# Optimization experiments

Measured on AMD Instinct MI355X. Metric: run time of the kernel, lower is better.

Reference implementation:

```python
import jax, jax.numpy as jnp
import numpy as np
from jax import lax

B, C, H, W = 8, 128, 256, 256
OUT_CH = 64
IN_CH = C * 9  # 1152: module's in_channels = 9 * image channels (unfold with 3x3 kernel)


def setup_inputs() -> dict:
    key = jax.random.key(0)
    k1, k2, k3 = jax.random.split(key, 3)
    x = jax.random.normal(k1, (B, C, H, W), dtype=jnp.float32)
    style = jax.random.normal(k2, (B, IN_CH), dtype=jnp.float32)
    # learned parameter: torch.randn(out_channels, in_channels, 1, 1) -> store as (out, in)
    weight = jax.random.normal(k3, (OUT_CH, IN_CH), dtype=jnp.float32)
    return {"x": x, "style": style, "weight": weight}


def reference(x, style, weight):
    b, c, h, w = x.shape
    out_ch, in_ch = weight.shape  # in_ch == c * 9
    # unfold column ordering is (c, kh, kw), so the flattened weight is exactly a
    # 3x3 conv kernel: (out, c*9) -> (out, c, 3, 3)
    w33 = weight.reshape(out_ch, c, 3, 3)
    # style.view(B,1,in_ch,1,1) * weight -> per-sample modulated 3x3 kernels
    w_mod = style.reshape(b, 1, c, 3, 3) * w33[None]  # (B, out, c, 3, 3)

    def conv_one(xi, wi):
        # xi: (c, h, w), wi: (out, c, 3, 3); SAME padding matches padding=(1,1)
        return lax.conv_general_dilated(
            xi[None], wi, window_strides=(1, 1), padding="SAME",
            dimension_numbers=("NCHW", "OIHW", "NCHW"))[0]

    out = jax.vmap(conv_one)(x, w_mod)  # (B, out, h, w)
    return out
```

## Files before the change

### kernel.cpp

```cpp
#include <hip/hip_runtime.h>
#include <hip/hip_bf16.h>

#define BATCH 8
#define CIN   128
#define HH    256
#define WW    256
#define OUTC  64
#define INCH  1152
#define HW    (HH*WW)
#define WMOD_BYTES ((size_t)BATCH * 9 * OUTC * CIN * 2)

typedef __attribute__((ext_vector_type(8)))  short short8;
typedef __attribute__((ext_vector_type(4)))  float f32x4;
typedef __attribute__((ext_vector_type(16))) float f32x16;

__device__ __forceinline__ unsigned short bf16r(float f) {
    unsigned u = __builtin_bit_cast(unsigned, f);
    u += 0x7fffu + ((u >> 16) & 1u);
    return (unsigned short)(u >> 16);
}

__global__ void __launch_bounds__(256) wmod_kernel(const float* __restrict__ weight,
                                                   const float* __restrict__ style,
                                                   unsigned short* __restrict__ wmod) {
    int i = blockIdx.x * 256 + threadIdx.x;
    if (i >= BATCH * 9 * OUTC * CIN) return;
    int c    = i & (CIN - 1);
    int rest = i >> 7;
    int o    = rest & (OUTC - 1);
    int bt   = rest >> 6;
    int tap  = bt % 9;
    int b    = bt / 9;
    int k    = c * 9 + tap;
    wmod[i] = bf16r(weight[o * INCH + k] * style[b * INCH + k]);
}

#define PBAR()                                              \
    do {                                                    \
        asm volatile("s_waitcnt lgkmcnt(0)" ::: "memory");  \
        __builtin_amdgcn_sched_barrier(0);                  \
        __builtin_amdgcn_s_barrier();                       \
        __builtin_amdgcn_sched_barrier(0);                  \
    } while (0)

template <bool GW>
__global__ void __launch_bounds__(256, 2) conv10_kernel(
    const float* __restrict__ x,
    const unsigned short* __restrict__ wmod,
    const float* __restrict__ weight,
    const float* __restrict__ style,
    float* __restrict__ out)
{
    __shared__ __align__(16) unsigned short xs_sm[2][340 * 20];

    const int tid = threadIdx.x;
    const int bx  = blockIdx.x;
    const int b   = blockIdx.y;
    const int h0  = (bx >> 3) * 8;
    const int w0  = (bx & 7) * 32;

    const int wv  = tid >> 6;
    const int l31 = tid & 31;
    const int kh2 = (tid >> 5) & 1;

    const bool tv = tid < 200;
    const int tt  = tv ? tid : 0;
    const int cg  = tt / 100;
    const int rem = tt % 100;
    const int sr  = rem / 10;
    const int qw  = rem % 10;
    const int sh  = h0 - 1 + sr;
    const bool hok = tv && ((unsigned)sh < HH);
    const int wl  = w0 - 4 + qw * 4;
    const int wlc = min(max(wl, 0), WW - 4);
    const int colbase = wl - (w0 - 1);
    const float* xbase = x + ((size_t)(b * CIN + cg * 8)) * HW +
                         (hok ? sh : 0) * WW + wlc;

    f32x4  f[8];
    short8 A[9][2];

    auto loadG = [&](int chunk) {
        if (hok) {
#pragma unroll
            for (int j = 0; j < 8; ++j)
                f[j] = *(const f32x4*)(xbase + (size_t)(chunk * 16 + j) * HW);
        }
    };

    auto writeG = [&](unsigned short* buf) {
        if (tv) {
#pragma unroll
            for (int u = 0; u < 4; ++u) {
                int col = colbase + u;
                if (col >= 0 && col < 34) {
                    bool wok = hok && ((unsigned)(wl + u) < WW);
                    short8 sv;
#pragma unroll
                    for (int j = 0; j < 8; ++j)
                        sv[j] = wok ? (short)bf16r(f[j][u]) : (short)0;
                    int s = sr * 34 + col;
                    *(short8*)&buf[s * 20 + cg * 8] = sv;
                }
            }
        }
    };

    auto loadA = [&](int chunk) {
        if (GW) {
            const unsigned short* wb =
                wmod + ((size_t)(b * 9) * OUTC) * CIN + chunk * 16 + kh2 * 8;
#pragma unroll
            for (int tap = 0; tap < 9; ++tap)
#pragma unroll
                for (int mi = 0; mi < 2; ++mi)
                    A[tap][mi] = *(const short8*)(
                        wb + ((size_t)tap * OUTC + mi * 32 + l31) * CIN);
        } else {
#pragma unroll
            for (int tap = 0; tap < 9; ++tap)
#pragma unroll
                for (int mi = 0; mi < 2; ++mi) {
                    int o = mi * 32 + l31;
#pragma unroll
                    for (int j = 0; j < 8; ++j) {
                        int c = chunk * 16 + kh2 * 8 + j;
                        int k = c * 9 + tap;
                        A[tap][mi][j] = (short)bf16r(weight[o * INCH + k] *
                                                     style[b * INCH + k]);
                    }
                }
        }
    };

    f32x16 acc[2][2];
#pragma unroll
    for (int mi = 0; mi < 2; ++mi)
#pragma unroll
        for (int ni = 0; ni < 2; ++ni)
#pragma unroll
            for (int r = 0; r < 16; ++r) acc[mi][ni][r] = 0.f;

    auto compute = [&](const unsigned short* buf) {
#pragma unroll
        for (int kh = 0; kh < 3; ++kh)
#pragma unroll
            for (int kw = 0; kw < 3; ++kw) {
                const int tap = kh * 3 + kw;
                short8 Bv[2];
#pragma unroll
                for (int ni = 0; ni < 2; ++ni) {
                    int s = (2 * wv + ni + kh) * 34 + l31 + kw;
                    Bv[ni] = *(const short8*)&buf[s * 20 + kh2 * 8];
                }
#pragma unroll
                for (int mi = 0; mi < 2; ++mi)
#pragma unroll
                    for (int ni = 0; ni < 2; ++ni)
                        acc[mi][ni] = __builtin_amdgcn_mfma_f32_32x32x16_bf16(
                            A[tap][mi], Bv[ni], acc[mi][ni], 0, 0, 0);
            }
    };

    loadG(0);
    loadA(0);
    __builtin_amdgcn_sched_barrier(0);
    writeG(xs_sm[0]);
    PBAR();

#pragma unroll
    for (int k = 0; k < 8; ++k) {
        if (k < 7) loadG(k + 1);
        __builtin_amdgcn_sched_barrier(0);
        compute(xs_sm[k & 1]);
        __builtin_amdgcn_sched_barrier(0);
        if (k < 7) {
            loadA(k + 1);
            writeG(xs_sm[(k & 1) ^ 1]);
            PBAR();
        }
    }

    float* op = out + ((size_t)b * OUTC) * HW + w0 + l31;
#pragma unroll
    for (int mi = 0; mi < 2; ++mi)
#pragma unroll
        for (int ni = 0; ni < 2; ++ni) {
            int h = h0 + 2 * wv + ni;
#pragma unroll
            for (int r = 0; r < 16; ++r) {
                int o = mi * 32 + (r & 3) + 8 * (r >> 2) + 4 * kh2;
                op[(size_t)o * HW + h * WW] = acc[mi][ni][r];
            }
        }
}

extern "C" void kernel_launch(void* const* d_in, const int* in_sizes, int n_in,
                              void* d_out, int out_size, void* d_ws, size_t ws_size,
                              hipStream_t stream) {
    const float* x      = (const float*)d_in[0];
    const float* style  = (const float*)d_in[1];
    const float* weight = (const float*)d_in[2];
    float* out = (float*)d_out;

    const int wmod_total = BATCH * 9 * OUTC * CIN;

    if (ws_size >= WMOD_BYTES) {
        unsigned short* wmodp = (unsigned short*)d_ws;
        wmod_kernel<<<(wmod_total + 255) / 256, 256, 0, stream>>>(weight, style, wmodp);
        conv10_kernel<true><<<dim3(256, BATCH), 256, 0, stream>>>(
            x, wmodp, nullptr, nullptr, out);
    } else {
        conv10_kernel<false><<<dim3(256, BATCH), 256, 0, stream>>>(
            x, nullptr, weight, style, out);
    }
}
```

Baseline: 229.2 us.

## Pre-pack input to bf16 channel-grouped layout and stage tiles via direct global-to-LDS loads

Adds a repack kernel that converts x to bf16 in a layout of 8-channel groups per pixel, then a new conv kernel that stages halo tiles straight into LDS with global_load_lds, pointing out-of-bounds pixels at a zeroed buffer. This removes the per-iteration fp32 loads, bf16 conversion and LDS writes from the conv's inner loop, and relaxes the barrier wait so only older loads must finish. In exchange it needs a large workspace and an extra full pass over x: a 256 MB fp32 read plus a 128 MB bf16 write and re-read. That traffic may cost more than the conv saves.

```diff
diff --git a/kernel.cpp b/kernel.cpp
--- a/kernel.cpp
+++ b/kernel.cpp
@@ -8,17 +8,40 @@
 #define OUTC  64
 #define INCH  1152
 #define HW    (HH*WW)
+
+#define PLANE_PX   ((size_t)HH * WW)
+#define PLANE_B    (PLANE_PX * 16)
+#define XG_BYTES   ((size_t)BATCH * 16 * PLANE_B)
 #define WMOD_BYTES ((size_t)BATCH * 9 * OUTC * CIN * 2)
+#define Z_BYTES    64
 
 typedef __attribute__((ext_vector_type(8)))  short short8;
 typedef __attribute__((ext_vector_type(4)))  float f32x4;
+typedef __attribute__((ext_vector_type(2)))  float f32x2;
 typedef __attribute__((ext_vector_type(16))) float f32x16;
+typedef __attribute__((ext_vector_type(4)))  unsigned int u32x4;
 
 __device__ __forceinline__ unsigned short bf16r(float f) {
     unsigned u = __builtin_bit_cast(unsigned, f);
     u += 0x7fffu + ((u >> 16) & 1u);
     return (unsigned short)(u >> 16);
 }
+
+__device__ __forceinline__ void gload16(const void* src, void* dst_lds) {
+    __builtin_amdgcn_global_load_lds(
+        (const __attribute__((address_space(1))) unsigned int*)src,
+        (__attribute__((address_space(3))) unsigned int*)dst_lds,
+        16, 0, 0);
+}
+
+#define PBAR18()                                                        \
+    do {                                                                \
+        __builtin_amdgcn_sched_barrier(0);                              \
+        asm volatile("s_waitcnt vmcnt(18) lgkmcnt(0)" ::: "memory");    \
+        __builtin_amdgcn_sched_barrier(0);                              \
+        __builtin_amdgcn_s_barrier();                                   \
+        __builtin_amdgcn_sched_barrier(0);                              \
+    } while (0)
 
 __global__ void __launch_bounds__(256) wmod_kernel(const float* __restrict__ weight,
                                                    const float* __restrict__ style,
@@ -35,7 +58,159 @@
     wmod[i] = bf16r(weight[o * INCH + k] * style[b * INCH + k]);
 }
 
-#define PBAR()                                              \
+__global__ void __launch_bounds__(256) repack_kernel(const float* __restrict__ x,
+                                                     unsigned short* __restrict__ xG) {
+    const int w2 = blockIdx.x * 128 + (threadIdx.x & 63) * 2;
+    const int cq = threadIdx.x >> 6;
+    const int h  = blockIdx.y;
+    const int b  = blockIdx.z;
+
+    const float* xp = x + ((size_t)(b * CIN + cq * 32)) * HW + h * WW + w2;
+
+    f32x2 f[32];
+#pragma unroll
+    for (int j = 0; j < 32; ++j) f[j] = *(const f32x2*)(xp + (size_t)j * HW);
+
+#pragma unroll
+    for (int g = 0; g < 4; ++g) {
+        int p = cq * 4 + g;
+        unsigned short* op =
+            xG + ((size_t)(b * 16 + p) * PLANE_PX + (size_t)h * WW + w2) * 8;
+#pragma unroll
+        for (int u = 0; u < 2; ++u) {
+            unsigned pk[4];
+#pragma unroll
+            for (int d = 0; d < 4; ++d)
+                pk[d] = (unsigned)bf16r(f[8 * g + 2 * d][u]) |
+                        ((unsigned)bf16r(f[8 * g + 2 * d + 1][u]) << 16);
+            u32x4 v = {pk[0], pk[1], pk[2], pk[3]};
+            *(u32x4*)(op + u * 8) = v;
+        }
+    }
+}
+
+__global__ void __launch_bounds__(256, 2) conv11_kernel(
+    const unsigned short* __restrict__ xG,
+    const unsigned short* __restrict__ wmod,
+    const unsigned short* __restrict__ zptr,
+    float* __restrict__ out)
+{
+    __shared__ __align__(16) unsigned short xs_sm[2][2 * 384 * 8];
+
+    const int tid = threadIdx.x;
+    const int bx  = blockIdx.x;
+    const int b   = blockIdx.y;
+    const int h0  = (bx >> 3) * 8;
+    const int w0  = (bx & 7) * 32;
+
+    const int wv    = tid >> 6;
+    const int l31   = tid & 31;
+    const int ghalf = (tid >> 5) & 1;
+
+    int  sg2[3];
+    size_t spx[3];
+    bool sok[3];
+#pragma unroll
+    for (int i = 0; i < 3; ++i) {
+        int G  = tid + i * 256;
+        int g2 = (G >= 384) ? 1 : 0;
+        int s  = G - g2 * 384;
+        int r   = s / 34;
+        int col = s - r * 34;
+        int h = h0 - 1 + r, w = w0 - 1 + col;
+        sok[i] = (s < 340) && ((unsigned)h < HH) && ((unsigned)w < WW);
+        sg2[i] = g2;
+        spx[i] = (size_t)((h & 255) * WW + (w & 255)) * 16;
+    }
+
+    const char* xGb = (const char*)xG + (size_t)b * 16 * PLANE_B;
+    const unsigned short* wmb = wmod + ((size_t)(b * 9) * OUTC) * CIN;
+
+    short8 A[9][2];
+
+    auto stage = [&](int k, int bufsel) {
+        char* base = (char*)&xs_sm[bufsel][0];
+#pragma unroll
+        for (int i = 0; i < 3; ++i) {
+            const void* src = sok[i]
+                ? (const void*)(xGb + (size_t)(2 * k + sg2[i]) * PLANE_B + spx[i])
+                : (const void*)zptr;
+            gload16(src, base + (size_t)(tid + i * 256) * 16);
+        }
+    };
+
+    auto loadA = [&](int k) {
+        const unsigned short* wb = wmb + k * 16 + ghalf * 8;
+#pragma unroll
+        for (int tap = 0; tap < 9; ++tap)
+#pragma unroll
+            for (int mi = 0; mi < 2; ++mi)
+                A[tap][mi] = *(const short8*)(
+                    wb + ((size_t)tap * OUTC + mi * 32 + l31) * CIN);
+    };
+
+    f32x16 acc[2][2];
+#pragma unroll
+    for (int mi = 0; mi < 2; ++mi)
+#pragma unroll
+        for (int ni = 0; ni < 2; ++ni)
+#pragma unroll
+            for (int r = 0; r < 16; ++r) acc[mi][ni][r] = 0.f;
+
+    auto compute = [&](int bufsel) {
+        const unsigned short* buf = &xs_sm[bufsel][0];
+        const int gb = ghalf * 384 * 8;
+#pragma unroll
+        for (int kh = 0; kh < 3; ++kh)
+#pragma unroll
+            for (int kw = 0; kw < 3; ++kw) {
+                const int tap = kh * 3 + kw;
+                short8 Bv[2];
+#pragma unroll
+                for (int ni = 0; ni < 2; ++ni) {
+                    int s = (2 * wv + ni + kh) * 34 + l31 + kw;
+                    Bv[ni] = *(const short8*)&buf[gb + s * 8];
+                }
+#pragma unroll
+                for (int mi = 0; mi < 2; ++mi)
+#pragma unroll
+                    for (int ni = 0; ni < 2; ++ni)
+                        acc[mi][ni] = __builtin_amdgcn_mfma_f32_32x32x16_bf16(
+                            A[tap][mi], Bv[ni], acc[mi][ni], 0, 0, 0);
+            }
+    };
+
+    stage(0, 0);
+    loadA(0);
+    PBAR18();
+
+#pragma unroll
+    for (int k = 0; k < 8; ++k) {
+        if (k < 7) stage(k + 1, (k + 1) & 1);
+        __builtin_amdgcn_sched_barrier(0);
+        compute(k & 1);
+        __builtin_amdgcn_sched_barrier(0);
+        if (k < 7) {
+            loadA(k + 1);
+            PBAR18();
+        }
+    }
+
+    float* op = out + ((size_t)b * OUTC) * HW + w0 + l31;
+#pragma unroll
+    for (int mi = 0; mi < 2; ++mi)
+#pragma unroll
+        for (int ni = 0; ni < 2; ++ni) {
+            int h = h0 + 2 * wv + ni;
+#pragma unroll
+            for (int r = 0; r < 16; ++r) {
+                int o = mi * 32 + (r & 3) + 8 * (r >> 2) + 4 * ghalf;
+                op[(size_t)o * HW + h * WW] = acc[mi][ni][r];
+            }
+        }
+}
+
+#define PBARL()                                             \
     do {                                                    \
         asm volatile("s_waitcnt lgkmcnt(0)" ::: "memory");  \
         __builtin_amdgcn_sched_barrier(0);                  \
@@ -87,7 +262,6 @@
                 f[j] = *(const f32x4*)(xbase + (size_t)(chunk * 16 + j) * HW);
         }
     };
-
     auto writeG = [&](unsigned short* buf) {
         if (tv) {
 #pragma unroll
@@ -105,7 +279,6 @@
             }
         }
     };
-
     auto loadA = [&](int chunk) {
         if (GW) {
             const unsigned short* wb =
@@ -166,7 +339,7 @@
     loadA(0);
     __builtin_amdgcn_sched_barrier(0);
     writeG(xs_sm[0]);
-    PBAR();
+    PBARL();
 
 #pragma unroll
     for (int k = 0; k < 8; ++k) {
@@ -177,7 +350,7 @@
         if (k < 7) {
             loadA(k + 1);
             writeG(xs_sm[(k & 1) ^ 1]);
-            PBAR();
+            PBARL();
         }
     }
 
@@ -205,7 +378,16 @@
 
     const int wmod_total = BATCH * 9 * OUTC * CIN;
 
-    if (ws_size >= WMOD_BYTES) {
+    if (ws_size >= XG_BYTES + WMOD_BYTES + Z_BYTES) {
+        unsigned short* xG    = (unsigned short*)d_ws;
+        unsigned short* wmodp = (unsigned short*)((char*)d_ws + XG_BYTES);
+        unsigned short* zptr  = (unsigned short*)((char*)d_ws + XG_BYTES + WMOD_BYTES);
+
+        wmod_kernel<<<(wmod_total + 255) / 256, 256, 0, stream>>>(weight, style, wmodp);
+        hipMemsetAsync(zptr, 0, Z_BYTES, stream);
+        repack_kernel<<<dim3(2, HH, BATCH), 256, 0, stream>>>(x, xG);
+        conv11_kernel<<<dim3(256, BATCH), 256, 0, stream>>>(xG, wmodp, zptr, out);
+    } else if (ws_size >= WMOD_BYTES) {
         unsigned short* wmodp = (unsigned short*)d_ws;
         wmod_kernel<<<(wmod_total + 255) / 256, 256, 0, stream>>>(weight, style, wmodp);
         conv10_kernel<true><<<dim3(256, BATCH), 256, 0, stream>>>(
```

Result: slower. 260.3 us (+13.6%).
